# Kernel tuning notes

Hardware: AMD Instinct MI355X
Metric: run time of the kernel (lower is better)

Reference implementation:

```python
import jax, jax.numpy as jnp
import numpy as np

EPS = 1e-16  # PyG softmax eps
NEG_SLOPE = 0.2


def _gat_conv(x, W, att_src, att_dst, bias, src, dst, num_nodes, heads, ch, concat):
    # add self loops (PyG default add_self_loops=True)
    loop = jnp.arange(num_nodes, dtype=src.dtype)
    src = jnp.concatenate([src, loop])
    dst = jnp.concatenate([dst, loop])

    h = (x @ W).reshape(num_nodes, heads, ch)          # [N,H,C]
    a_src = jnp.sum(h * att_src, axis=-1)              # [N,H]
    a_dst = jnp.sum(h * att_dst, axis=-1)              # [N,H]

    e = a_src[src] + a_dst[dst]                        # [E,H]
    e = jnp.where(e > 0, e, NEG_SLOPE * e)             # leaky_relu

    # segment softmax over edges grouped by destination node
    m = jax.ops.segment_max(e, dst, num_segments=num_nodes)
    e = jnp.exp(e - m[dst])
    s = jax.ops.segment_sum(e, dst, num_segments=num_nodes)
    alpha = e / (s[dst] + EPS)                          # [E,H]

    msg = h[src] * alpha[:, :, None]                    # [E,H,C]
    out = jax.ops.segment_sum(msg, dst, num_segments=num_nodes)  # [N,H,C]

    if concat:
        out = out.reshape(num_nodes, heads * ch)
    else:
        out = out.mean(axis=1)
    return out + bias


def setup_inputs() -> dict:
    key = jax.random.key(0)
    ks = jax.random.split(key, 12)
    N, E = 50000, 800000
    C_in, C_hid, C_out, H = 128, 32, 64, 8

    x = jax.random.normal(ks[0], (N, C_in), dtype=jnp.float32)
    edge_index = jax.random.randint(ks[1], (2, E), 0, N, dtype=jnp.int64)
    edge_weight = jax.random.uniform(ks[2], (E,), dtype=jnp.float32)

    g = lambda k, shape, fan: jax.random.normal(k, shape, dtype=jnp.float32) * (1.0 / np.sqrt(fan))
    W1 = g(ks[3], (C_in, H * C_hid), C_in)
    att_src1 = g(ks[4], (H, C_hid), C_hid)
    att_dst1 = g(ks[5], (H, C_hid), C_hid)
    bias1 = jnp.zeros((H * C_hid,), dtype=jnp.float32)
    W2 = g(ks[6], (H * C_hid, C_out), H * C_hid)
    att_src2 = g(ks[7], (1, C_out), C_out)
    att_dst2 = g(ks[8], (1, C_out), C_out)
    bias2 = jnp.zeros((C_out,), dtype=jnp.float32)

    return {"x": x, "edge_index": edge_index, "edge_weight": edge_weight,
            "W1": W1, "att_src1": att_src1, "att_dst1": att_dst1, "bias1": bias1,
            "W2": W2, "att_src2": att_src2, "att_dst2": att_dst2, "bias2": bias2}


def reference(x, edge_index, edge_weight, W1, att_src1, att_dst1, bias1,
              W2, att_src2, att_dst2, bias2):
    N = x.shape[0]
    src, dst = edge_index[0], edge_index[1]
    # edge_weight is ignored: GATConv has edge_dim=None, so edge_attr contributes nothing
    h = _gat_conv(x, W1, att_src1, att_dst1, bias1, src, dst, N, 8, 32, concat=True)
    h = jax.nn.elu(h)
    out = _gat_conv(h, W2, att_src2, att_dst2, bias2, src, dst, N, 1, 64, concat=False)
    return out
```

## Files before the change

kernel.cpp:

```cpp
#include <hip/hip_runtime.h>
#include <hip/hip_fp16.h>
#include <math.h>


#define LEAKY(e) ((e) > 0.f ? (e) : 0.2f * (e))
#define CAP 64
#define NPB 12500
#define NPART 4
#define CS 8192

struct __align__(8) H4 { __half2 a, b; };

typedef _Float16 half8 __attribute__((ext_vector_type(8)));
typedef float f32x4 __attribute__((ext_vector_type(4)));

__global__ __launch_bounds__(256) void k1_kernel(
    const int* __restrict__ ei, unsigned* __restrict__ Hg,
    const float* __restrict__ x,
    const float* __restrict__ W1, _Float16* __restrict__ h1h,
    const float* __restrict__ att_src1, const float* __restrict__ att_dst1,
    float* __restrict__ a_src1, float* __restrict__ a_dst1, int N, int E,
    int B, int hblocks) {
  __shared__ __align__(16) unsigned sraw[NPB];
  int t = threadIdx.x, b = blockIdx.x;
  if (b < hblocks) {
    int chunk = b >> 2, p = b & 3;
    for (int i = t; i < NPB; i += 256) sraw[i] = 0u;
    __syncthreads();
    int base = chunk * CS;
    int pbase = p * NPB;
    for (int j = 0; j < CS; j += 256) {
      int idx = base + j + t;
      if (idx < E) {
        int d = ei[E + idx];
        unsigned dl = (unsigned)(d - pbase);
        if (dl < NPB) atomicAdd(&sraw[dl], 1u);
      }
    }
    __syncthreads();
    unsigned* Hs = Hg + (size_t)(p * B + chunk) * NPB;
    for (int i = t; i < NPB; i += 256) Hs[i] = sraw[i];
    return;
  }
  _Float16* Bs = (_Float16*)sraw;
  int bx = b - hblocks;
  int cb = bx & 3;
  int c0 = cb * 64;
  int w = t >> 6, l = t & 63;
  int lm = l & 15, lq = l >> 4;
  {
    int n = t & 63;
    int kw = t >> 6;
#pragma unroll 8
    for (int i = 0; i < 32; i++) {
      int k = i * 4 + kw;
      Bs[n * 136 + k] = (_Float16)W1[k * 256 + c0 + n];
    }
  }
  __syncthreads();
  int m0 = (bx >> 2) * 128 + w * 32;
  int ra = m0 + lm;      if (ra > N - 1) ra = N - 1;
  int rb = m0 + 16 + lm; if (rb > N - 1) rb = N - 1;
  f32x4 acc[2][4];
#pragma unroll
  for (int mt = 0; mt < 2; mt++)
#pragma unroll
    for (int nt = 0; nt < 4; nt++) acc[mt][nt] = (f32x4){0.f, 0.f, 0.f, 0.f};
  for (int k0 = 0; k0 < 128; k0 += 32) {
    const float* pa = x + (size_t)ra * 128 + k0 + lq * 8;
    const float* pb = x + (size_t)rb * 128 + k0 + lq * 8;
    float4 u0 = *(const float4*)pa, u1 = *(const float4*)(pa + 4);
    float4 w0 = *(const float4*)pb, w1 = *(const float4*)(pb + 4);
    half8 a0, a1;
    a0[0] = (_Float16)u0.x; a0[1] = (_Float16)u0.y;
    a0[2] = (_Float16)u0.z; a0[3] = (_Float16)u0.w;
    a0[4] = (_Float16)u1.x; a0[5] = (_Float16)u1.y;
    a0[6] = (_Float16)u1.z; a0[7] = (_Float16)u1.w;
    a1[0] = (_Float16)w0.x; a1[1] = (_Float16)w0.y;
    a1[2] = (_Float16)w0.z; a1[3] = (_Float16)w0.w;
    a1[4] = (_Float16)w1.x; a1[5] = (_Float16)w1.y;
    a1[6] = (_Float16)w1.z; a1[7] = (_Float16)w1.w;
    half8 b0 = *(const half8*)(Bs + (0 + lm) * 136 + k0 + lq * 8);
    half8 b1 = *(const half8*)(Bs + (16 + lm) * 136 + k0 + lq * 8);
    half8 b2 = *(const half8*)(Bs + (32 + lm) * 136 + k0 + lq * 8);
    half8 b3 = *(const half8*)(Bs + (48 + lm) * 136 + k0 + lq * 8);
    acc[0][0] = __builtin_amdgcn_mfma_f32_16x16x32_f16(a0, b0, acc[0][0], 0, 0, 0);
    acc[0][1] = __builtin_amdgcn_mfma_f32_16x16x32_f16(a0, b1, acc[0][1], 0, 0, 0);
    acc[0][2] = __builtin_amdgcn_mfma_f32_16x16x32_f16(a0, b2, acc[0][2], 0, 0, 0);
    acc[0][3] = __builtin_amdgcn_mfma_f32_16x16x32_f16(a0, b3, acc[0][3], 0, 0, 0);
    acc[1][0] = __builtin_amdgcn_mfma_f32_16x16x32_f16(a1, b0, acc[1][0], 0, 0, 0);
    acc[1][1] = __builtin_amdgcn_mfma_f32_16x16x32_f16(a1, b1, acc[1][1], 0, 0, 0);
    acc[1][2] = __builtin_amdgcn_mfma_f32_16x16x32_f16(a1, b2, acc[1][2], 0, 0, 0);
    acc[1][3] = __builtin_amdgcn_mfma_f32_16x16x32_f16(a1, b3, acc[1][3], 0, 0, 0);
  }
  float as_[4], ad_[4];
#pragma unroll
  for (int nt = 0; nt < 4; nt++) {
    as_[nt] = att_src1[c0 + nt * 16 + lm];
    ad_[nt] = att_dst1[c0 + nt * 16 + lm];
  }
#pragma unroll
  for (int mt = 0; mt < 2; mt++) {
#pragma unroll
    for (int i = 0; i < 4; i++) {
      int gr = m0 + mt * 16 + lq * 4 + i;
      bool ok = gr < N;
      if (ok) {
#pragma unroll
        for (int nt = 0; nt < 4; nt++)
          h1h[(size_t)gr * 256 + c0 + nt * 16 + lm] = (_Float16)acc[mt][nt][i];
      }
      float p0 = acc[mt][0][i] * as_[0] + acc[mt][1][i] * as_[1];
      float p1 = acc[mt][2][i] * as_[2] + acc[mt][3][i] * as_[3];
      float q0 = acc[mt][0][i] * ad_[0] + acc[mt][1][i] * ad_[1];
      float q1 = acc[mt][2][i] * ad_[2] + acc[mt][3][i] * ad_[3];
#pragma unroll
      for (int o = 1; o < 16; o <<= 1) {
        p0 += __shfl_xor(p0, o, 64);
        p1 += __shfl_xor(p1, o, 64);
        q0 += __shfl_xor(q0, o, 64);
        q1 += __shfl_xor(q1, o, 64);
      }
      if (lm == 0 && ok) {
        int h0 = c0 >> 5;
        a_src1[(size_t)gr * 8 + h0] = p0;
        a_src1[(size_t)gr * 8 + h0 + 1] = p1;
        a_dst1[(size_t)gr * 8 + h0] = q0;
        a_dst1[(size_t)gr * 8 + h0 + 1] = q1;
      }
    }
  }
}

__global__ __launch_bounds__(256) void prefix_kernel(
    unsigned* __restrict__ Hg, int* __restrict__ deg,
    int* __restrict__ csr_src, int N, int B) {
  int d = blockIdx.x * 256 + threadIdx.x;
  if (d >= N) return;
  int p = d / NPB;
  int dl = d - p * NPB;
  unsigned* Hp = Hg + (size_t)p * B * NPB + dl;
  unsigned sum = 0u;
  for (int b = 0; b < B; b++) {
    unsigned v = Hp[(size_t)b * NPB];
    Hp[(size_t)b * NPB] = sum;
    sum += v;
  }
  deg[d] = (int)sum;
  csr_src[(size_t)d * CAP] = d;
}

__global__ __launch_bounds__(256) void scatter_kernel(
    const int* __restrict__ ei, const unsigned* __restrict__ Hg,
    int* __restrict__ csr_src, int E, int B) {
  __shared__ unsigned cnt[NPB];
  int t = threadIdx.x, b = blockIdx.x;
  int chunk = b >> 2, p = b & 3;
  for (int i = t; i < NPB; i += 256) cnt[i] = 0u;
  __syncthreads();
  int base = chunk * CS;
  int pbase = p * NPB;
  const unsigned* Hs = Hg + (size_t)(p * B + chunk) * NPB;
  for (int j = 0; j < CS; j += 256) {
    int idx = base + j + t;
    if (idx < E) {
      int s = ei[idx];
      int d = ei[E + idx];
      unsigned dl = (unsigned)(d - pbase);
      if (dl < NPB) {
        unsigned local = atomicAdd(&cnt[dl], 1u);
        unsigned pos = Hs[dl];
        int slot = 1 + (int)(pos + local);
        if (slot < CAP) csr_src[(size_t)d * CAP + slot] = s;
      }
    }
  }
}

__global__ __launch_bounds__(256) void agg1_kernel(
    const int* __restrict__ deg, const int* __restrict__ csr_src,
    const float* __restrict__ a_src1, const float* __restrict__ a_dst1,
    const __half* __restrict__ h1h, const float* __restrict__ bias,
    _Float16* __restrict__ h_act, int n) {
  int w = threadIdx.x >> 6, l = threadIdx.x & 63;
  int d = blockIdx.x * 4 + w;
  if (d >= n) return;
  int cnt = deg[d] + 1;
  if (cnt > CAP) cnt = CAP;
  const int* sp = csr_src + (size_t)d * CAP;
  int hh = l >> 3;
  float adst = a_dst1[(size_t)d * 8 + hh];
  float4 acc = make_float4(0.f, 0.f, 0.f, 0.f);
  float p = 0.f;
  int i = 0;
  for (; i + 8 <= cnt; i += 8) {
    int s[8];
    H4 v[8];
    float xv[8];
#pragma unroll
    for (int j = 0; j < 8; j++) s[j] = sp[i + j];
#pragma unroll
    for (int j = 0; j < 8; j++)
      v[j] = *(const H4*)(h1h + (size_t)s[j] * 256 + 4 * l);
#pragma unroll
    for (int j = 0; j < 8; j++) {
      float e = a_src1[(size_t)s[j] * 8 + hh] + adst;
      e = LEAKY(e);
      xv[j] = __expf(e);
      p += xv[j];
    }
#pragma unroll
    for (int j = 0; j < 8; j++) {
      float2 p0 = __half22float2(v[j].a), p1 = __half22float2(v[j].b);
      acc.x = fmaf(p0.x, xv[j], acc.x);
      acc.y = fmaf(p0.y, xv[j], acc.y);
      acc.z = fmaf(p1.x, xv[j], acc.z);
      acc.w = fmaf(p1.y, xv[j], acc.w);
    }
  }
  for (; i < cnt; i++) {
    int s = sp[i];
    float e = a_src1[(size_t)s * 8 + hh] + adst;
    e = LEAKY(e);
    float a = __expf(e);
    p += a;
    H4 v = *(const H4*)(h1h + (size_t)s * 256 + 4 * l);
    float2 p0 = __half22float2(v.a), p1 = __half22float2(v.b);
    acc.x = fmaf(p0.x, a, acc.x);
    acc.y = fmaf(p0.y, a, acc.y);
    acc.z = fmaf(p1.x, a, acc.z);
    acc.w = fmaf(p1.y, a, acc.w);
  }
  float rinv = 1.f / (p + 1e-16f);
  float4 b = *(const float4*)(bias + 4 * l);
  float ox = fmaf(acc.x, rinv, b.x), oy = fmaf(acc.y, rinv, b.y);
  float oz = fmaf(acc.z, rinv, b.z), ow = fmaf(acc.w, rinv, b.w);
  ox = ox > 0.f ? ox : expm1f(ox);
  oy = oy > 0.f ? oy : expm1f(oy);
  oz = oz > 0.f ? oz : expm1f(oz);
  ow = ow > 0.f ? ow : expm1f(ow);
  H4 hv;
  hv.a = __floats2half2_rn(ox, oy);
  hv.b = __floats2half2_rn(oz, ow);
  *(H4*)(h_act + (size_t)d * 256 + 4 * l) = hv;
}

__global__ __launch_bounds__(256) void gemm2_kernel(
    const _Float16* __restrict__ h_act, const float* __restrict__ W2,
    _Float16* __restrict__ h2h, const float* __restrict__ att_src2,
    const float* __restrict__ att_dst2, float* __restrict__ a_src2,
    float* __restrict__ a_dst2, int N) {
  __shared__ _Float16 Bs[64 * 264];
  int t = threadIdx.x;
  int w = t >> 6, l = t & 63;
  int lm = l & 15, lq = l >> 4;
  {
    int n = t & 63;
    int kw = t >> 6;
#pragma unroll 8
    for (int i = 0; i < 64; i++) {
      int k = i * 4 + kw;
      Bs[n * 264 + k] = (_Float16)W2[k * 64 + n];
    }
  }
  __syncthreads();
  const int K = 256;
  int m0 = blockIdx.x * 128 + w * 32;
  int ra = m0 + lm;      if (ra > N - 1) ra = N - 1;
  int rb = m0 + 16 + lm; if (rb > N - 1) rb = N - 1;
  f32x4 acc[2][4];
#pragma unroll
  for (int mt = 0; mt < 2; mt++)
#pragma unroll
    for (int nt = 0; nt < 4; nt++) acc[mt][nt] = (f32x4){0.f, 0.f, 0.f, 0.f};
  for (int k0 = 0; k0 < K; k0 += 32) {
    half8 a0 = *(const half8*)(h_act + (size_t)ra * K + k0 + lq * 8);
    half8 a1 = *(const half8*)(h_act + (size_t)rb * K + k0 + lq * 8);
    half8 b0 = *(const half8*)(Bs + (0 + lm) * 264 + k0 + lq * 8);
    half8 b1 = *(const half8*)(Bs + (16 + lm) * 264 + k0 + lq * 8);
    half8 b2 = *(const half8*)(Bs + (32 + lm) * 264 + k0 + lq * 8);
    half8 b3 = *(const half8*)(Bs + (48 + lm) * 264 + k0 + lq * 8);
    acc[0][0] = __builtin_amdgcn_mfma_f32_16x16x32_f16(a0, b0, acc[0][0], 0, 0, 0);
    acc[0][1] = __builtin_amdgcn_mfma_f32_16x16x32_f16(a0, b1, acc[0][1], 0, 0, 0);
    acc[0][2] = __builtin_amdgcn_mfma_f32_16x16x32_f16(a0, b2, acc[0][2], 0, 0, 0);
    acc[0][3] = __builtin_amdgcn_mfma_f32_16x16x32_f16(a0, b3, acc[0][3], 0, 0, 0);
    acc[1][0] = __builtin_amdgcn_mfma_f32_16x16x32_f16(a1, b0, acc[1][0], 0, 0, 0);
    acc[1][1] = __builtin_amdgcn_mfma_f32_16x16x32_f16(a1, b1, acc[1][1], 0, 0, 0);
    acc[1][2] = __builtin_amdgcn_mfma_f32_16x16x32_f16(a1, b2, acc[1][2], 0, 0, 0);
    acc[1][3] = __builtin_amdgcn_mfma_f32_16x16x32_f16(a1, b3, acc[1][3], 0, 0, 0);
  }
  float as_[4], ad_[4];
#pragma unroll
  for (int nt = 0; nt < 4; nt++) {
    as_[nt] = att_src2[nt * 16 + lm];
    ad_[nt] = att_dst2[nt * 16 + lm];
  }
#pragma unroll
  for (int mt = 0; mt < 2; mt++) {
#pragma unroll
    for (int i = 0; i < 4; i++) {
      int gr = m0 + mt * 16 + lq * 4 + i;
      bool ok = gr < N;
      if (ok) {
#pragma unroll
        for (int nt = 0; nt < 4; nt++)
          h2h[(size_t)gr * 64 + nt * 16 + lm] = (_Float16)acc[mt][nt][i];
      }
      float p0 = acc[mt][0][i] * as_[0] + acc[mt][1][i] * as_[1];
      float p1 = acc[mt][2][i] * as_[2] + acc[mt][3][i] * as_[3];
      float q0 = acc[mt][0][i] * ad_[0] + acc[mt][1][i] * ad_[1];
      float q1 = acc[mt][2][i] * ad_[2] + acc[mt][3][i] * ad_[3];
#pragma unroll
      for (int o = 1; o < 16; o <<= 1) {
        p0 += __shfl_xor(p0, o, 64);
        p1 += __shfl_xor(p1, o, 64);
        q0 += __shfl_xor(q0, o, 64);
        q1 += __shfl_xor(q1, o, 64);
      }
      if (lm == 0 && ok) {
        a_src2[gr] = p0 + p1;
        a_dst2[gr] = q0 + q1;
      }
    }
  }
}

__global__ __launch_bounds__(256) void agg2_kernel(
    const int* __restrict__ deg, const int* __restrict__ csr_src,
    const float* __restrict__ a_src2, const float* __restrict__ a_dst2,
    const __half* __restrict__ h2h, const float* __restrict__ bias,
    float* __restrict__ out, int n) {
  int w = threadIdx.x >> 6, l = threadIdx.x & 63;
  int d = blockIdx.x * 4 + w;
  if (d >= n) return;
  int cnt = deg[d] + 1;
  if (cnt > CAP) cnt = CAP;
  const int* sp = csr_src + (size_t)d * CAP;
  float adst = a_dst2[d];
  int e2 = l >> 5;
  int c2 = (l & 31) * 2;
  float2 acc = make_float2(0.f, 0.f);
  float p = 0.f;
  int i = 0;
  for (; i + 16 <= cnt; i += 16) {
    int s[8];
    __half2 v[8];
    float xv[8];
#pragma unroll
    for (int j = 0; j < 8; j++) s[j] = sp[i + j * 2 + e2];
#pragma unroll
    for (int j = 0; j < 8; j++)
      v[j] = *(const __half2*)(h2h + (size_t)s[j] * 64 + c2);
#pragma unroll
    for (int j = 0; j < 8; j++) {
      float e = a_src2[s[j]] + adst;
      e = LEAKY(e);
      xv[j] = __expf(e);
      p += xv[j];
    }
#pragma unroll
    for (int j = 0; j < 8; j++) {
      float2 f = __half22float2(v[j]);
      acc.x = fmaf(f.x, xv[j], acc.x);
      acc.y = fmaf(f.y, xv[j], acc.y);
    }
  }
  for (; i + e2 < cnt; i += 2) {
    int s = sp[i + e2];
    float e = a_src2[s] + adst;
    e = LEAKY(e);
    float a = __expf(e);
    p += a;
    float2 f = __half22float2(*(const __half2*)(h2h + (size_t)s * 64 + c2));
    acc.x = fmaf(f.x, a, acc.x);
    acc.y = fmaf(f.y, a, acc.y);
  }
  acc.x += __shfl_xor(acc.x, 32, 64);
  acc.y += __shfl_xor(acc.y, 32, 64);
  p += __shfl_xor(p, 32, 64);
  if (l < 32) {
    float rinv = 1.f / (p + 1e-16f);
    float2 b = *(const float2*)(bias + c2);
    *(float2*)(out + (size_t)d * 64 + c2) =
        make_float2(fmaf(acc.x, rinv, b.x), fmaf(acc.y, rinv, b.y));
  }
}

extern "C" void kernel_launch(void* const* d_in, const int* in_sizes, int n_in,
                              void* d_out, int out_size, void* d_ws, size_t ws_size,
                              hipStream_t stream) {
  const float* x        = (const float*)d_in[0];
  const int*   ei       = (const int*)d_in[1];
  const float* W1       = (const float*)d_in[3];
  const float* att_src1 = (const float*)d_in[4];
  const float* att_dst1 = (const float*)d_in[5];
  const float* bias1    = (const float*)d_in[6];
  const float* W2       = (const float*)d_in[7];
  const float* att_src2 = (const float*)d_in[8];
  const float* att_dst2 = (const float*)d_in[9];
  const float* bias2    = (const float*)d_in[10];
  float* out = (float*)d_out;

  int N = in_sizes[0] / 128;
  int E = in_sizes[1] / 2;

  char* ws = (char*)d_ws;
  size_t off = 0;
  auto carve = [&](size_t bytes) -> void* {
    void* p = ws + off;
    off += (bytes + 255) & ~(size_t)255;
    return p;
  };
  _Float16* h1h   = (_Float16*)carve((size_t)N * 256 * 2);
  _Float16* h2h   = (_Float16*)carve((size_t)N * 64 * 2);
  _Float16* h_act = (_Float16*)carve((size_t)N * 256 * 2);
  float* a_src1  = (float*)carve((size_t)N * 8 * 4);
  float* a_dst1  = (float*)carve((size_t)N * 8 * 4);
  float* a_src2  = (float*)carve((size_t)N * 4);
  float* a_dst2  = (float*)carve((size_t)N * 4);
  int* deg       = (int*)carve((size_t)N * 4);
  int* csr_src   = (int*)carve((size_t)N * CAP * 4);
  (void)ws_size; (void)n_in; (void)out_size;

  int B = (E + CS - 1) / CS;
  int hblocks = B * NPART;
  unsigned* Hg = (unsigned*)h_act;

  int gblocks = ((N + 127) / 128) * 4;
  k1_kernel<<<hblocks + gblocks, 256, 0, stream>>>(
      ei, Hg, x, W1, h1h, att_src1, att_dst1, a_src1, a_dst1, N, E, B,
      hblocks);
  prefix_kernel<<<(N + 255) / 256, 256, 0, stream>>>(Hg, deg, csr_src, N, B);
  scatter_kernel<<<hblocks, 256, 0, stream>>>(ei, Hg, csr_src, E, B);
  agg1_kernel<<<(N + 3) / 4, 256, 0, stream>>>(
      deg, csr_src, a_src1, a_dst1, (const __half*)h1h, bias1, h_act, N);
  gemm2_kernel<<<(N + 127) / 128, 256, 0, stream>>>(
      h_act, W2, h2h, att_src2, att_dst2, a_src2, a_dst2, N);
  agg2_kernel<<<(N + 3) / 4, 256, 0, stream>>>(
      deg, csr_src, a_src2, a_dst2, (const __half*)h2h, bias2, out, N);
}
```

Before: 303.5 us.

## Pack histogram counters into 16-bit halves and use persistent aggregation loops

The per-chunk destination histogram now packs two 16-bit counters per 32-bit shared word. This halves the number of partitions and histogram blocks, and halves the prefix-scan work and global histogram traffic. The scatter kernel seeds its shared counters with the prefix offsets, so one atomic returns the final slot directly. Both aggregation kernels become grid-stride loops over a fixed 2048 blocks, and their remainder loops are replaced by clamped, masked 8-wide batches. Risks are 16-bit counter overflow if a chunk holds 65536 or more edges to one node, and wasted lanes on the masked tail batches.

```diff
diff --git a/kernel.cpp b/kernel.cpp
--- a/kernel.cpp
+++ b/kernel.cpp
@@ -5,9 +5,10 @@
 
 #define LEAKY(e) ((e) > 0.f ? (e) : 0.2f * (e))
 #define CAP 64
-#define NPB 12500
-#define NPART 4
-#define CS 8192
+#define NPART 2
+#define NPB 25000
+#define NPW 12500
+#define CS 16384
 
 struct __align__(8) H4 { __half2 a, b; };
 
@@ -21,11 +22,11 @@
     const float* __restrict__ att_src1, const float* __restrict__ att_dst1,
     float* __restrict__ a_src1, float* __restrict__ a_dst1, int N, int E,
     int B, int hblocks) {
-  __shared__ __align__(16) unsigned sraw[NPB];
+  __shared__ __align__(16) unsigned sraw[NPW];
   int t = threadIdx.x, b = blockIdx.x;
   if (b < hblocks) {
-    int chunk = b >> 2, p = b & 3;
-    for (int i = t; i < NPB; i += 256) sraw[i] = 0u;
+    int chunk = b >> 1, p = b & 1;
+    for (int i = t; i < NPW; i += 256) sraw[i] = 0u;
     __syncthreads();
     int base = chunk * CS;
     int pbase = p * NPB;
@@ -34,12 +35,12 @@
       if (idx < E) {
         int d = ei[E + idx];
         unsigned dl = (unsigned)(d - pbase);
-        if (dl < NPB) atomicAdd(&sraw[dl], 1u);
+        if (dl < NPB) atomicAdd(&sraw[dl >> 1], 1u << ((dl & 1) * 16));
       }
     }
     __syncthreads();
-    unsigned* Hs = Hg + (size_t)(p * B + chunk) * NPB;
-    for (int i = t; i < NPB; i += 256) Hs[i] = sraw[i];
+    unsigned* Hs = Hg + (size_t)(p * B + chunk) * NPW;
+    for (int i = t; i < NPW; i += 256) Hs[i] = sraw[i];
     return;
   }
   _Float16* Bs = (_Float16*)sraw;
@@ -135,32 +136,33 @@
 __global__ __launch_bounds__(256) void prefix_kernel(
     unsigned* __restrict__ Hg, int* __restrict__ deg,
     int* __restrict__ csr_src, int N, int B) {
-  int d = blockIdx.x * 256 + threadIdx.x;
-  if (d >= N) return;
-  int p = d / NPB;
-  int dl = d - p * NPB;
-  unsigned* Hp = Hg + (size_t)p * B * NPB + dl;
-  unsigned sum = 0u;
+  int wid = blockIdx.x * 256 + threadIdx.x;
+  if (wid >= NPART * NPW) return;
+  int p = wid / NPW, w0 = wid - p * NPW;
+  unsigned* Hp = Hg + (size_t)p * B * NPW + w0;
+  unsigned lo = 0, hi = 0;
   for (int b = 0; b < B; b++) {
-    unsigned v = Hp[(size_t)b * NPB];
-    Hp[(size_t)b * NPB] = sum;
-    sum += v;
-  }
-  deg[d] = (int)sum;
-  csr_src[(size_t)d * CAP] = d;
+    unsigned v = Hp[(size_t)b * NPW];
+    Hp[(size_t)b * NPW] = lo | (hi << 16);
+    lo += v & 0xffffu;
+    hi += v >> 16;
+  }
+  int d0 = p * NPB + 2 * w0, d1 = d0 + 1;
+  if (d0 < N) { deg[d0] = (int)lo; csr_src[(size_t)d0 * CAP] = d0; }
+  if (d1 < N) { deg[d1] = (int)hi; csr_src[(size_t)d1 * CAP] = d1; }
 }
 
 __global__ __launch_bounds__(256) void scatter_kernel(
     const int* __restrict__ ei, const unsigned* __restrict__ Hg,
     int* __restrict__ csr_src, int E, int B) {
-  __shared__ unsigned cnt[NPB];
+  __shared__ unsigned cnt[NPW];
   int t = threadIdx.x, b = blockIdx.x;
-  int chunk = b >> 2, p = b & 3;
-  for (int i = t; i < NPB; i += 256) cnt[i] = 0u;
+  int chunk = b >> 1, p = b & 1;
+  const unsigned* Hs = Hg + (size_t)(p * B + chunk) * NPW;
+  for (int i = t; i < NPW; i += 256) cnt[i] = Hs[i];
   __syncthreads();
   int base = chunk * CS;
   int pbase = p * NPB;
-  const unsigned* Hs = Hg + (size_t)(p * B + chunk) * NPB;
   for (int j = 0; j < CS; j += 256) {
     int idx = base + j + t;
     if (idx < E) {
@@ -168,9 +170,9 @@
       int d = ei[E + idx];
       unsigned dl = (unsigned)(d - pbase);
       if (dl < NPB) {
-        unsigned local = atomicAdd(&cnt[dl], 1u);
-        unsigned pos = Hs[dl];
-        int slot = 1 + (int)(pos + local);
+        unsigned sh = (dl & 1) * 16;
+        unsigned old = atomicAdd(&cnt[dl >> 1], 1u << sh);
+        int slot = 1 + (int)((old >> sh) & 0xffffu);
         if (slot < CAP) csr_src[(size_t)d * CAP + slot] = s;
       }
     }
@@ -183,66 +185,57 @@
     const __half* __restrict__ h1h, const float* __restrict__ bias,
     _Float16* __restrict__ h_act, int n) {
   int w = threadIdx.x >> 6, l = threadIdx.x & 63;
-  int d = blockIdx.x * 4 + w;
-  if (d >= n) return;
-  int cnt = deg[d] + 1;
-  if (cnt > CAP) cnt = CAP;
-  const int* sp = csr_src + (size_t)d * CAP;
   int hh = l >> 3;
-  float adst = a_dst1[(size_t)d * 8 + hh];
-  float4 acc = make_float4(0.f, 0.f, 0.f, 0.f);
-  float p = 0.f;
-  int i = 0;
-  for (; i + 8 <= cnt; i += 8) {
-    int s[8];
-    H4 v[8];
-    float xv[8];
-#pragma unroll
-    for (int j = 0; j < 8; j++) s[j] = sp[i + j];
-#pragma unroll
-    for (int j = 0; j < 8; j++)
-      v[j] = *(const H4*)(h1h + (size_t)s[j] * 256 + 4 * l);
-#pragma unroll
-    for (int j = 0; j < 8; j++) {
-      float e = a_src1[(size_t)s[j] * 8 + hh] + adst;
-      e = LEAKY(e);
-      xv[j] = __expf(e);
-      p += xv[j];
-    }
-#pragma unroll
-    for (int j = 0; j < 8; j++) {
-      float2 p0 = __half22float2(v[j].a), p1 = __half22float2(v[j].b);
-      acc.x = fmaf(p0.x, xv[j], acc.x);
-      acc.y = fmaf(p0.y, xv[j], acc.y);
-      acc.z = fmaf(p1.x, xv[j], acc.z);
-      acc.w = fmaf(p1.y, xv[j], acc.w);
-    }
-  }
-  for (; i < cnt; i++) {
-    int s = sp[i];
-    float e = a_src1[(size_t)s * 8 + hh] + adst;
-    e = LEAKY(e);
-    float a = __expf(e);
-    p += a;
-    H4 v = *(const H4*)(h1h + (size_t)s * 256 + 4 * l);
-    float2 p0 = __half22float2(v.a), p1 = __half22float2(v.b);
-    acc.x = fmaf(p0.x, a, acc.x);
-    acc.y = fmaf(p0.y, a, acc.y);
-    acc.z = fmaf(p1.x, a, acc.z);
-    acc.w = fmaf(p1.y, a, acc.w);
-  }
-  float rinv = 1.f / (p + 1e-16f);
-  float4 b = *(const float4*)(bias + 4 * l);
-  float ox = fmaf(acc.x, rinv, b.x), oy = fmaf(acc.y, rinv, b.y);
-  float oz = fmaf(acc.z, rinv, b.z), ow = fmaf(acc.w, rinv, b.w);
-  ox = ox > 0.f ? ox : expm1f(ox);
-  oy = oy > 0.f ? oy : expm1f(oy);
-  oz = oz > 0.f ? oz : expm1f(oz);
-  ow = ow > 0.f ? ow : expm1f(ow);
-  H4 hv;
-  hv.a = __floats2half2_rn(ox, oy);
-  hv.b = __floats2half2_rn(oz, ow);
-  *(H4*)(h_act + (size_t)d * 256 + 4 * l) = hv;
+  int c4 = 4 * l;
+  float4 bb = *(const float4*)(bias + c4);
+  int nw = gridDim.x * 4;
+  for (int d = blockIdx.x * 4 + w; d < n; d += nw) {
+    int cnt = deg[d] + 1;
+    if (cnt > CAP) cnt = CAP;
+    const int* sp = csr_src + (size_t)d * CAP;
+    float adst = a_dst1[(size_t)d * 8 + hh];
+    float4 acc = make_float4(0.f, 0.f, 0.f, 0.f);
+    float p = 0.f;
+    for (int i = 0; i < cnt; i += 8) {
+      int s[8];
+      H4 v[8];
+      float xv[8];
+#pragma unroll
+      for (int j = 0; j < 8; j++) {
+        int k = i + j;
+        s[j] = sp[k < cnt ? k : cnt - 1];
+      }
+#pragma unroll
+      for (int j = 0; j < 8; j++)
+        v[j] = *(const H4*)(h1h + (size_t)s[j] * 256 + c4);
+#pragma unroll
+      for (int j = 0; j < 8; j++) {
+        float e = a_src1[(size_t)s[j] * 8 + hh] + adst;
+        e = LEAKY(e);
+        xv[j] = (i + j < cnt) ? __expf(e) : 0.f;
+        p += xv[j];
+      }
+#pragma unroll
+      for (int j = 0; j < 8; j++) {
+        float2 p0 = __half22float2(v[j].a), p1 = __half22float2(v[j].b);
+        acc.x = fmaf(p0.x, xv[j], acc.x);
+        acc.y = fmaf(p0.y, xv[j], acc.y);
+        acc.z = fmaf(p1.x, xv[j], acc.z);
+        acc.w = fmaf(p1.y, xv[j], acc.w);
+      }
+    }
+    float rinv = 1.f / (p + 1e-16f);
+    float ox = fmaf(acc.x, rinv, bb.x), oy = fmaf(acc.y, rinv, bb.y);
+    float oz = fmaf(acc.z, rinv, bb.z), ow = fmaf(acc.w, rinv, bb.w);
+    ox = ox > 0.f ? ox : expm1f(ox);
+    oy = oy > 0.f ? oy : expm1f(oy);
+    oz = oz > 0.f ? oz : expm1f(oz);
+    ow = ow > 0.f ? ow : expm1f(ow);
+    H4 hv;
+    hv.a = __floats2half2_rn(ox, oy);
+    hv.b = __floats2half2_rn(oz, ow);
+    *(H4*)(h_act + (size_t)d * 256 + c4) = hv;
+  }
 }
 
 __global__ __launch_bounds__(256) void gemm2_kernel(
@@ -331,58 +324,51 @@
     const __half* __restrict__ h2h, const float* __restrict__ bias,
     float* __restrict__ out, int n) {
   int w = threadIdx.x >> 6, l = threadIdx.x & 63;
-  int d = blockIdx.x * 4 + w;
-  if (d >= n) return;
-  int cnt = deg[d] + 1;
-  if (cnt > CAP) cnt = CAP;
-  const int* sp = csr_src + (size_t)d * CAP;
-  float adst = a_dst2[d];
   int e2 = l >> 5;
   int c2 = (l & 31) * 2;
-  float2 acc = make_float2(0.f, 0.f);
-  float p = 0.f;
-  int i = 0;
-  for (; i + 16 <= cnt; i += 16) {
-    int s[8];
-    __half2 v[8];
-    float xv[8];
-#pragma unroll
-    for (int j = 0; j < 8; j++) s[j] = sp[i + j * 2 + e2];
-#pragma unroll
-    for (int j = 0; j < 8; j++)
-      v[j] = *(const __half2*)(h2h + (size_t)s[j] * 64 + c2);
-#pragma unroll
-    for (int j = 0; j < 8; j++) {
-      float e = a_src2[s[j]] + adst;
-      e = LEAKY(e);
-      xv[j] = __expf(e);
-      p += xv[j];
-    }
-#pragma unroll
-    for (int j = 0; j < 8; j++) {
-      float2 f = __half22float2(v[j]);
-      acc.x = fmaf(f.x, xv[j], acc.x);
-      acc.y = fmaf(f.y, xv[j], acc.y);
-    }
-  }
-  for (; i + e2 < cnt; i += 2) {
-    int s = sp[i + e2];
-    float e = a_src2[s] + adst;
-    e = LEAKY(e);
-    float a = __expf(e);
-    p += a;
-    float2 f = __half22float2(*(const __half2*)(h2h + (size_t)s * 64 + c2));
-    acc.x = fmaf(f.x, a, acc.x);
-    acc.y = fmaf(f.y, a, acc.y);
-  }
-  acc.x += __shfl_xor(acc.x, 32, 64);
-  acc.y += __shfl_xor(acc.y, 32, 64);
-  p += __shfl_xor(p, 32, 64);
-  if (l < 32) {
-    float rinv = 1.f / (p + 1e-16f);
-    float2 b = *(const float2*)(bias + c2);
-    *(float2*)(out + (size_t)d * 64 + c2) =
-        make_float2(fmaf(acc.x, rinv, b.x), fmaf(acc.y, rinv, b.y));
+  float2 bb = *(const float2*)(bias + c2);
+  int nw = gridDim.x * 4;
+  for (int d = blockIdx.x * 4 + w; d < n; d += nw) {
+    int cnt = deg[d] + 1;
+    if (cnt > CAP) cnt = CAP;
+    const int* sp = csr_src + (size_t)d * CAP;
+    float adst = a_dst2[d];
+    float2 acc = make_float2(0.f, 0.f);
+    float p = 0.f;
+    for (int i = 0; i < cnt; i += 16) {
+      int s[8];
+      __half2 v[8];
+      float xv[8];
+#pragma unroll
+      for (int j = 0; j < 8; j++) {
+        int k = i + j * 2 + e2;
+        s[j] = sp[k < cnt ? k : cnt - 1];
+      }
+#pragma unroll
+      for (int j = 0; j < 8; j++)
+        v[j] = *(const __half2*)(h2h + (size_t)s[j] * 64 + c2);
+#pragma unroll
+      for (int j = 0; j < 8; j++) {
+        float e = a_src2[s[j]] + adst;
+        e = LEAKY(e);
+        xv[j] = ((i + j * 2 + e2) < cnt) ? __expf(e) : 0.f;
+        p += xv[j];
+      }
+#pragma unroll
+      for (int j = 0; j < 8; j++) {
+        float2 f = __half22float2(v[j]);
+        acc.x = fmaf(f.x, xv[j], acc.x);
+        acc.y = fmaf(f.y, xv[j], acc.y);
+      }
+    }
+    float sx = acc.x + __shfl_xor(acc.x, 32, 64);
+    float sy = acc.y + __shfl_xor(acc.y, 32, 64);
+    float pp = p + __shfl_xor(p, 32, 64);
+    if (l < 32) {
+      float rinv = 1.f / (pp + 1e-16f);
+      *(float2*)(out + (size_t)d * 64 + c2) =
+          make_float2(fmaf(sx, rinv, bb.x), fmaf(sy, rinv, bb.y));
+    }
   }
 }
 
@@ -430,12 +416,13 @@
   k1_kernel<<<hblocks + gblocks, 256, 0, stream>>>(
       ei, Hg, x, W1, h1h, att_src1, att_dst1, a_src1, a_dst1, N, E, B,
       hblocks);
-  prefix_kernel<<<(N + 255) / 256, 256, 0, stream>>>(Hg, deg, csr_src, N, B);
+  int pwords = NPART * NPW;
+  prefix_kernel<<<(pwords + 255) / 256, 256, 0, stream>>>(Hg, deg, csr_src, N, B);
   scatter_kernel<<<hblocks, 256, 0, stream>>>(ei, Hg, csr_src, E, B);
-  agg1_kernel<<<(N + 3) / 4, 256, 0, stream>>>(
+  agg1_kernel<<<2048, 256, 0, stream>>>(
       deg, csr_src, a_src1, a_dst1, (const __half*)h1h, bias1, h_act, N);
   gemm2_kernel<<<(N + 127) / 128, 256, 0, stream>>>(
       h_act, W2, h2h, att_src2, att_dst2, a_src2, a_dst2, N);
-  agg2_kernel<<<(N + 3) / 4, 256, 0, stream>>>(
+  agg2_kernel<<<2048, 256, 0, stream>>>(
       deg, csr_src, a_src2, a_dst2, (const __half*)h2h, bias2, out, N);
 }
```

Result: slower. 357.8 us (+17.9%).
